# Kernel tuning notes

Measured on AMD Instinct MI355X. Metric: run time of the kernel, lower is better.

The kernel has to match this reference:

```python
import jax, jax.numpy as jnp
import numpy as np
import math

B, S_IMG, S_TXT = 1, 2048, 256
D_MODEL, HEADS, HEAD_DIM = 3072, 24, 128
INNER = HEADS * HEAD_DIM
EPS = 1e-6


def _rmsnorm(x, scale):
    # flax-style RMSNorm over last dim, fp32 stats
    x32 = x.astype(jnp.float32)
    var = jnp.mean(x32 * x32, axis=-1, keepdims=True)
    return ((x32 * jax.lax.rsqrt(var + EPS)).astype(x.dtype)) * scale


def _rope(x, cos, sin):
    # x: [B,S,H,D]; cos,sin: [S,D]; interleaved-pair rotation (use_real_unbind_dim=-1)
    c = cos[None, :, None, :].astype(jnp.float32)
    s = sin[None, :, None, :].astype(jnp.float32)
    xp = x.reshape(*x.shape[:-1], -1, 2)
    x_rot = jnp.stack([-xp[..., 1], xp[..., 0]], axis=-1).reshape(x.shape)
    return (x.astype(jnp.float32) * c + x_rot.astype(jnp.float32) * s).astype(x.dtype)


def setup_inputs() -> dict:
    key = jax.random.key(0)
    ks = jax.random.split(key, 16)
    w = lambda k, shp: jax.random.normal(k, shp, jnp.float32) * 0.02
    S = S_TXT + S_IMG
    pos = jnp.arange(S, dtype=jnp.float32)
    inv_freq = 1.0 / (10000.0 ** (jnp.arange(0, HEAD_DIM, 2, dtype=jnp.float32) / HEAD_DIM))
    ang = pos[:, None] * inv_freq[None, :]  # [S, D/2]
    cos = jnp.repeat(jnp.cos(ang), 2, axis=-1)  # [S, D] paired layout
    sin = jnp.repeat(jnp.sin(ang), 2, axis=-1)
    return {
        'hidden_states': jax.random.normal(ks[0], (B, S_IMG, D_MODEL), jnp.float32),
        'encoder_hidden_states': jax.random.normal(ks[1], (B, S_TXT, D_MODEL), jnp.float32),
        'cos': cos,
        'sin': sin,
        'wq': w(ks[2], (D_MODEL, INNER)),
        'wk': w(ks[3], (D_MODEL, INNER)),
        'wv': w(ks[4], (D_MODEL, INNER)),
        'wq_add': w(ks[5], (D_MODEL, INNER)),
        'wk_add': w(ks[6], (D_MODEL, INNER)),
        'wv_add': w(ks[7], (D_MODEL, INNER)),
        'bq_add': w(ks[8], (INNER,)),
        'bk_add': w(ks[9], (INNER,)),
        'bv_add': w(ks[10], (INNER,)),
        'norm_q': jnp.ones((HEAD_DIM,), jnp.float32),
        'norm_k': jnp.ones((HEAD_DIM,), jnp.float32),
        'norm_add_q': jnp.ones((HEAD_DIM,), jnp.float32),
        'norm_add_k': jnp.ones((HEAD_DIM,), jnp.float32),
        'w_out': w(ks[11], (INNER, D_MODEL)),
        'b_out': w(ks[12], (D_MODEL,)),
        'w_add_out': w(ks[13], (INNER, D_MODEL)),
        'b_add_out': w(ks[14], (D_MODEL,)),
    }


def reference(hidden_states, encoder_hidden_states, cos, sin, wq, wk, wv,
              wq_add, wk_add, wv_add, bq_add, bk_add, bv_add,
              norm_q, norm_k, norm_add_q, norm_add_k,
              w_out, b_out, w_add_out, b_add_out):
    St = encoder_hidden_states.shape[1]
    heads = lambda x: x.reshape(x.shape[0], x.shape[1], HEADS, HEAD_DIM)
    # image-token q/k/v + QK RMSNorm
    q = _rmsnorm(heads(hidden_states @ wq), norm_q)
    k = _rmsnorm(heads(hidden_states @ wk), norm_k)
    v = heads(hidden_states @ wv)
    # encoder-token q/k/v (biased projections) + QK RMSNorm
    eq = _rmsnorm(heads(encoder_hidden_states @ wq_add + bq_add), norm_add_q)
    ek = _rmsnorm(heads(encoder_hidden_states @ wk_add + bk_add), norm_add_k)
    ev = heads(encoder_hidden_states @ wv_add + bv_add)
    # encoder tokens concatenated first
    q = jnp.concatenate([eq, q], axis=1)
    k = jnp.concatenate([ek, k], axis=1)
    v = jnp.concatenate([ev, v], axis=1)
    q = _rope(q, cos, sin)
    k = _rope(k, cos, sin)
    # naive softmax attention
    scale = 1.0 / math.sqrt(HEAD_DIM)
    attn = jnp.einsum('bshd,bthd->bhst', q, k) * scale
    attn = jax.nn.softmax(attn, axis=-1)
    out = jnp.einsum('bhst,bthd->bshd', attn, v)
    out = out.reshape(out.shape[0], out.shape[1], -1)
    # split back into encoder / image streams and apply output projections
    enc_out = out[:, :St] @ w_add_out + b_add_out
    img_out = out[:, St:] @ w_out + b_out
    return (img_out, enc_out)
```

## Files before the change

kernel.cpp:

```cpp
#include <hip/hip_runtime.h>
#include <hip/hip_bf16.h>

typedef unsigned short u16;
typedef unsigned int   u32;
typedef __bf16 bf16x8 __attribute__((ext_vector_type(8)));
typedef float  f32x4  __attribute__((ext_vector_type(4)));

#define SEQ   2304
#define DM    3072
#define NH    24
#define HD    128
#define S_TXT 256
#define S_IMG 2048
#define SCALE 0.08838834764831845f

__device__ __forceinline__ u16 f2bf(float x) {
  u32 u = __float_as_uint(x);
  u += 0x7fffu + ((u >> 16) & 1u);
  return (u16)(u >> 16);
}
__device__ __forceinline__ float bf2f(u16 b) {
  return __uint_as_float(((u32)b) << 16);
}
__device__ __forceinline__ f32x4 zero4() { f32x4 z = {0.f, 0.f, 0.f, 0.f}; return z; }

#define GLDS16(gp, lp) __builtin_amdgcn_global_load_lds( \
    (__attribute__((address_space(1))) void*)(gp),       \
    (__attribute__((address_space(3))) void*)(lp), 16, 0, 0)

__global__ __launch_bounds__(256) void conv_bf16_k(const float* __restrict__ src,
                                                   u16* __restrict__ dst, int n4) {
  int i = blockIdx.x * 256 + threadIdx.x;
  if (i >= n4) return;
  float4 v = ((const float4*)src)[i];
  ushort4 o;
  o.x = f2bf(v.x); o.y = f2bf(v.y); o.z = f2bf(v.z); o.w = f2bf(v.w);
  ((ushort4*)dst)[i] = o;
}

struct WP { const float* s[8]; u16* d[8]; };

__global__ __launch_bounds__(256) void w_transpose_k(WP p) {
  __shared__ float tile[32][33];
  const float* __restrict__ src = p.s[blockIdx.z];
  u16* __restrict__ dst = p.d[blockIdx.z];
  const int c0 = blockIdx.x * 32, r0 = blockIdx.y * 32;
  const int tx = threadIdx.x & 31, ty = threadIdx.x >> 5;
#pragma unroll
  for (int i = 0; i < 4; ++i)
    tile[ty + i*8][tx] = src[(size_t)(r0 + ty + i*8) * DM + c0 + tx];
  __syncthreads();
#pragma unroll
  for (int i = 0; i < 4; ++i)
    dst[(size_t)(c0 + ty + i*8) * DM + r0 + tx] = f2bf(tile[tx][ty + i*8]);
}

__global__ __launch_bounds__(256) void v_transpose_k(const u16* __restrict__ V,
                                                     u16* __restrict__ Vt) {
  __shared__ u16 tile[32][34];
  const int h = blockIdx.z;
  const int t0 = blockIdx.x * 32, d0 = blockIdx.y * 32;
  const int tx = threadIdx.x & 31, ty = threadIdx.x >> 5;
#pragma unroll
  for (int i = 0; i < 4; ++i)
    tile[ty + i*8][tx] = V[((size_t)h * SEQ + t0 + ty + i*8) * HD + d0 + tx];
  __syncthreads();
#pragma unroll
  for (int i = 0; i < 4; ++i)
    Vt[((size_t)h * HD + d0 + ty + i*8) * SEQ + t0 + tx] = tile[tx][ty + i*8];
}

__global__ __launch_bounds__(256) void gemm_bt_k(
    const u16* __restrict__ A,
    const u16* __restrict__ B0, const u16* __restrict__ B1, const u16* __restrict__ B2,
    const float* __restrict__ bias0, const float* __restrict__ bias1, const float* __restrict__ bias2,
    void* __restrict__ out0, void* __restrict__ out1, void* __restrict__ out2,
    int row_off, int mode) {
  __shared__ __attribute__((aligned(128))) char As[128*128];
  __shared__ __attribute__((aligned(128))) char Bs[128*128];
  const int bz = blockIdx.z;
  const u16* __restrict__ Bm = (bz == 0) ? B0 : ((bz == 1) ? B1 : B2);
  const float* __restrict__ bias = (bz == 0) ? bias0 : ((bz == 1) ? bias1 : bias2);
  void* out = (bz == 0) ? out0 : ((bz == 1) ? out1 : out2);
  const int bm = blockIdx.x, bn = blockIdx.y;
  const int tid = threadIdx.x;
  const int w = tid >> 6, l = tid & 63;
  const int wr = w >> 1, wc = w & 1;

  f32x4 acc[4][4];
#pragma unroll
  for (int mi = 0; mi < 4; ++mi)
#pragma unroll
    for (int ni = 0; ni < 4; ++ni) acc[mi][ni] = zero4();

  const int srow  = l >> 3;
  const int scolb = ((l & 7) ^ srow) << 4;
  const char* Ag = (const char*)(A  + (size_t)(bm*128 + w*32) * DM) + (size_t)srow * (DM*2) + scolb;
  const char* Bg = (const char*)(Bm + (size_t)(bn*128 + w*32) * DM) + (size_t)srow * (DM*2) + scolb;
  char* AsW = As + (w*32) * 128;
  char* BsW = Bs + (w*32) * 128;

  for (int kt = 0; kt < DM/64; ++kt) {
#pragma unroll
    for (int i = 0; i < 4; ++i) {
      GLDS16(Ag + (size_t)i*8*(DM*2) + kt*128, AsW + i*8*128);
      GLDS16(Bg + (size_t)i*8*(DM*2) + kt*128, BsW + i*8*128);
    }
    __syncthreads();
#pragma unroll
    for (int kk = 0; kk < 2; ++kk) {
      bf16x8 af[4], bfr[4];
#pragma unroll
      for (int mi = 0; mi < 4; ++mi) {
        const int row = wr*64 + mi*16 + (l & 15);
        const int cb  = ((kk << 6) + ((l >> 4) << 4)) ^ ((row & 7) << 4);
        af[mi] = *(const bf16x8*)(As + row*128 + cb);
      }
#pragma unroll
      for (int ni = 0; ni < 4; ++ni) {
        const int row = wc*64 + ni*16 + (l & 15);
        const int cb  = ((kk << 6) + ((l >> 4) << 4)) ^ ((row & 7) << 4);
        bfr[ni] = *(const bf16x8*)(Bs + row*128 + cb);
      }
#pragma unroll
      for (int mi = 0; mi < 4; ++mi)
#pragma unroll
        for (int ni = 0; ni < 4; ++ni)
          acc[mi][ni] = __builtin_amdgcn_mfma_f32_16x16x32_bf16(af[mi], bfr[ni], acc[mi][ni], 0, 0, 0);
    }
    __syncthreads();
  }

#pragma unroll
  for (int mi = 0; mi < 4; ++mi) {
    const int mbase = bm*128 + wr*64 + mi*16 + ((l >> 4) << 2);
#pragma unroll
    for (int ni = 0; ni < 4; ++ni) {
      const int ncol = bn*128 + wc*64 + ni*16 + (l & 15);
      const float bv = bias ? bias[ncol] : 0.f;
#pragma unroll
      for (int r = 0; r < 4; ++r) {
        const float v = acc[mi][ni][r] + bv;
        if (mode == 0) {
          ((u16*)out)[((size_t)bn * SEQ + (row_off + mbase + r)) * HD + (ncol & 127)] = f2bf(v);
        } else {
          ((float*)out)[(size_t)(mbase + r) * DM + ncol] = v;
        }
      }
    }
  }
}

__global__ __launch_bounds__(256) void qk_norm_rope_k(
    const u16* __restrict__ Qf, const u16* __restrict__ Kf,
    u16* __restrict__ Qb, u16* __restrict__ Kb,
    const float* __restrict__ cosT, const float* __restrict__ sinT,
    const float* __restrict__ nq, const float* __restrict__ nk,
    const float* __restrict__ naq, const float* __restrict__ nak) {
  const int gw = (blockIdx.x * 256 + threadIdx.x) >> 6;
  const int l = threadIdx.x & 63;
  const int which = (gw >= NH * SEQ) ? 1 : 0;
  const int rem = which ? (gw - NH * SEQ) : gw;
  const int h = rem / SEQ, t = rem % SEQ;
  const size_t base = ((size_t)h * SEQ + t) * HD + l * 2;
  const ushort2 xb = *(const ushort2*)((which ? Kf : Qf) + base);
  const float x0 = bf2f(xb.x), x1 = bf2f(xb.y);
  float ss = x0*x0 + x1*x1;
#pragma unroll
  for (int msk = 1; msk < 64; msk <<= 1) ss += __shfl_xor(ss, msk, 64);
  const float rr = rsqrtf(ss * (1.0f/128.0f) + 1e-6f);
  const float* nw = which ? (t < S_TXT ? nak : nk) : (t < S_TXT ? naq : nq);
  const float n0 = x0 * rr * nw[l*2], n1 = x1 * rr * nw[l*2 + 1];
  const float c = cosT[(size_t)t * HD + l*2], sn = sinT[(size_t)t * HD + l*2];
  float o0 = n0 * c - n1 * sn;
  float o1 = n1 * c + n0 * sn;
  if (!which) { o0 *= SCALE; o1 *= SCALE; }
  ushort2 ob; ob.x = f2bf(o0); ob.y = f2bf(o1);
  *(ushort2*)((which ? Kb : Qb) + base) = ob;
}

__global__ __launch_bounds__(256) void attn_k(
    const u16* __restrict__ Q, const u16* __restrict__ K,
    const u16* __restrict__ Vt, u16* __restrict__ O) {
  __shared__ __attribute__((aligned(128))) char Kl[64*256];
  __shared__ __attribute__((aligned(128))) char Vl[128*128];
  __shared__ __attribute__((aligned(128))) char Pl[4][2048];
  const int qt = blockIdx.x, h = blockIdx.y;
  const int tid = threadIdx.x, w = tid >> 6, l = tid & 63;

  const u16* Qh = Q  + ((size_t)h * SEQ + qt*64 + w*16) * HD;
  const u16* Kh = K  + (size_t)h * SEQ * HD;
  const u16* Vh = Vt + (size_t)h * HD * SEQ;

  bf16x8 qf[4];
#pragma unroll
  for (int kf = 0; kf < 4; ++kf)
    qf[kf] = *(const bf16x8*)(Qh + (l & 15) * HD + kf*32 + ((l >> 4) << 3));

  f32x4 o[8];
#pragma unroll
  for (int db = 0; db < 8; ++db) o[db] = zero4();
  float m[4]  = {-1e30f, -1e30f, -1e30f, -1e30f};
  float rl[4] = {0.f, 0.f, 0.f, 0.f};

  const int vswz = ((l & 7) ^ (l >> 3)) << 4;

  for (int kb = 0; kb < SEQ/64; ++kb) {
#pragma unroll
    for (int i = 0; i < 4; ++i) {
      const int rloc = i*4 + (l >> 4);
      const int colb = ((l & 15) << 4) ^ ((rloc & 7) << 4);
      GLDS16((const char*)Kh + ((size_t)(kb*64 + w*16 + rloc)) * 256 + colb,
             Kl + (w*16 + i*4) * 256);
    }
#pragma unroll
    for (int i = 0; i < 4; ++i) {
      const int rloc = w*32 + i*8 + (l >> 3);
      GLDS16((const char*)Vh + (size_t)rloc * (SEQ*2) + kb*128 + vswz,
             Vl + (w*32 + i*8) * 128);
    }
    __syncthreads();

    f32x4 s[4];
#pragma unroll
    for (int ni = 0; ni < 4; ++ni) {
      f32x4 a = zero4();
      const int row = ni*16 + (l & 15);
#pragma unroll
      for (int kf = 0; kf < 4; ++kf) {
        const int cb = ((kf << 6) + ((l >> 4) << 4)) ^ ((row & 7) << 4);
        bf16x8 kfr = *(const bf16x8*)(Kl + row*256 + cb);
        a = __builtin_amdgcn_mfma_f32_16x16x32_bf16(qf[kf], kfr, a, 0, 0, 0);
      }
      s[ni] = a;
    }

    float mnew[4], resc[4];
#pragma unroll
    for (int r = 0; r < 4; ++r) {
      float mx = fmaxf(fmaxf(s[0][r], s[1][r]), fmaxf(s[2][r], s[3][r]));
#pragma unroll
      for (int msk = 1; msk < 16; msk <<= 1) mx = fmaxf(mx, __shfl_xor(mx, msk, 64));
      mnew[r] = fmaxf(m[r], mx);
      resc[r] = __expf(m[r] - mnew[r]);
      m[r] = mnew[r];
    }
#pragma unroll
    for (int ni = 0; ni < 4; ++ni) {
      f32x4 t = s[ni];
#pragma unroll
      for (int r = 0; r < 4; ++r) t[r] = __expf(t[r] - m[r]);
      s[ni] = t;
    }
#pragma unroll
    for (int r = 0; r < 4; ++r) {
      float t = s[0][r] + s[1][r] + s[2][r] + s[3][r];
#pragma unroll
      for (int msk = 1; msk < 16; msk <<= 1) t += __shfl_xor(t, msk, 64);
      rl[r] = rl[r] * resc[r] + t;
    }
#pragma unroll
    for (int db = 0; db < 8; ++db) {
      f32x4 t = o[db];
#pragma unroll
      for (int r = 0; r < 4; ++r) t[r] *= resc[r];
      o[db] = t;
    }

    char* Pw = Pl[w];
#pragma unroll
    for (int ni = 0; ni < 4; ++ni)
#pragma unroll
      for (int r = 0; r < 4; ++r) {
        const int prow = ((l >> 4) << 2) + r;
        const int pcb  = ((ni*16 + (l & 15)) << 1) ^ ((prow & 7) << 4);
        *(u16*)(Pw + prow*128 + pcb) = f2bf(s[ni][r]);
      }

    const int arow = l & 15;
#pragma unroll
    for (int kblk = 0; kblk < 2; ++kblk) {
      const int pcb = ((kblk << 6) + ((l >> 4) << 4)) ^ ((arow & 7) << 4);
      bf16x8 pa = *(const bf16x8*)(Pw + arow*128 + pcb);
#pragma unroll
      for (int db = 0; db < 8; ++db) {
        const int vrow = db*16 + (l & 15);
        const int vcb  = ((kblk << 6) + ((l >> 4) << 4)) ^ ((vrow & 7) << 4);
        bf16x8 vb = *(const bf16x8*)(Vl + vrow*128 + vcb);
        o[db] = __builtin_amdgcn_mfma_f32_16x16x32_bf16(pa, vb, o[db], 0, 0, 0);
      }
    }
    __syncthreads();
  }

#pragma unroll
  for (int r = 0; r < 4; ++r) rl[r] = 1.f / rl[r];
#pragma unroll
  for (int db = 0; db < 8; ++db)
#pragma unroll
    for (int r = 0; r < 4; ++r) {
      const int token = qt*64 + w*16 + ((l >> 4) << 2) + r;
      const int col = h*HD + db*16 + (l & 15);
      O[(size_t)token * DM + col] = f2bf(o[db][r] * rl[r]);
    }
}

extern "C" void kernel_launch(void* const* d_in, const int* in_sizes, int n_in,
                              void* d_out, int out_size, void* d_ws, size_t ws_size,
                              hipStream_t stream) {
  const float* hidden = (const float*)d_in[0];
  const float* ench   = (const float*)d_in[1];
  const float* cosT   = (const float*)d_in[2];
  const float* sinT   = (const float*)d_in[3];
  const float* wq  = (const float*)d_in[4];
  const float* wk  = (const float*)d_in[5];
  const float* wv  = (const float*)d_in[6];
  const float* wqa = (const float*)d_in[7];
  const float* wka = (const float*)d_in[8];
  const float* wva = (const float*)d_in[9];
  const float* bqa = (const float*)d_in[10];
  const float* bka = (const float*)d_in[11];
  const float* bva = (const float*)d_in[12];
  const float* nq  = (const float*)d_in[13];
  const float* nk  = (const float*)d_in[14];
  const float* naq = (const float*)d_in[15];
  const float* nak = (const float*)d_in[16];
  const float* w_out     = (const float*)d_in[17];
  const float* b_out     = (const float*)d_in[18];
  const float* w_add_out = (const float*)d_in[19];
  const float* b_add_out = (const float*)d_in[20];
  float* outp = (float*)d_out;
  (void)in_sizes; (void)n_in; (void)out_size; (void)ws_size;

  char* ws = (char*)d_ws;
  size_t off = 0;
  auto alloc = [&](size_t n) { char* p = ws + off; off += (n + 255) & ~(size_t)255; return p; };
  u16* wt[8];
  for (int i = 0; i < 8; ++i) wt[i] = (u16*)alloc((size_t)DM * DM * 2);
  u16* xb_img = (u16*)alloc((size_t)S_IMG * DM * 2);
  u16* xb_enc = (u16*)alloc((size_t)S_TXT * DM * 2);
  u16* Qf = (u16*)alloc((size_t)NH * SEQ * HD * 2);
  u16* Kf = (u16*)alloc((size_t)NH * SEQ * HD * 2);
  u16* Vf = (u16*)alloc((size_t)NH * SEQ * HD * 2);
  u16* Qb = (u16*)alloc((size_t)NH * SEQ * HD * 2);
  u16* Kb = (u16*)alloc((size_t)NH * SEQ * HD * 2);
  u16* Vt = (u16*)alloc((size_t)NH * HD * SEQ * 2);
  u16* Ob = (u16*)alloc((size_t)SEQ * DM * 2);

  conv_bf16_k<<<(S_IMG*DM/4)/256, 256, 0, stream>>>(hidden, xb_img, S_IMG*DM/4);
  conv_bf16_k<<<(S_TXT*DM/4)/256, 256, 0, stream>>>(ench, xb_enc, S_TXT*DM/4);

  WP wp;
  wp.s[0] = wq;  wp.s[1] = wk;  wp.s[2] = wv;
  wp.s[3] = wqa; wp.s[4] = wka; wp.s[5] = wva;
  wp.s[6] = w_out; wp.s[7] = w_add_out;
  for (int i = 0; i < 8; ++i) wp.d[i] = wt[i];
  w_transpose_k<<<dim3(96, 96, 8), 256, 0, stream>>>(wp);

  gemm_bt_k<<<dim3(16, 24, 3), 256, 0, stream>>>(xb_img, wt[0], wt[1], wt[2],
      nullptr, nullptr, nullptr, Qf, Kf, Vf, S_TXT, 0);
  gemm_bt_k<<<dim3(2, 24, 3), 256, 0, stream>>>(xb_enc, wt[3], wt[4], wt[5],
      bqa, bka, bva, Qf, Kf, Vf, 0, 0);

  qk_norm_rope_k<<<(2*NH*SEQ)/4, 256, 0, stream>>>(Qf, Kf, Qb, Kb, cosT, sinT, nq, nk, naq, nak);
  v_transpose_k<<<dim3(SEQ/32, HD/32, NH), 256, 0, stream>>>(Vf, Vt);

  attn_k<<<dim3(SEQ/64, NH), 256, 0, stream>>>(Qb, Kb, Vt, Ob);

  gemm_bt_k<<<dim3(16, 24, 1), 256, 0, stream>>>(Ob + (size_t)S_TXT * DM, wt[6], wt[6], wt[6],
      b_out, b_out, b_out, outp, outp, outp, 0, 1);
  gemm_bt_k<<<dim3(2, 24, 1), 256, 0, stream>>>(Ob, wt[7], wt[7], wt[7],
      b_add_out, b_add_out, b_add_out,
      outp + (size_t)S_IMG * DM, outp + (size_t)S_IMG * DM, outp + (size_t)S_IMG * DM, 0, 1);
}
```

Before: 939.7 us.

## Process two query tiles per wave in attention to reuse K/V LDS loads

Each wave now handles 32 query rows (two 16-row tiles) instead of 16, so each block covers 128 queries and the grid is halved. Every K and V fragment read from LDS now feeds two MFMAs. QK^T is computed transposed (K as the A operand), so the row max and row sum need only two cross-lane shuffles. P is packed with v_cvt_pk_bf16_f32. This cuts LDS and global K/V traffic per query but raises register pressure, and the smaller grid (18x24 blocks) may lower occupancy and CU fill.

```diff
diff --git a/kernel.cpp b/kernel.cpp
--- a/kernel.cpp
+++ b/kernel.cpp
@@ -23,6 +23,11 @@
   return __uint_as_float(((u32)b) << 16);
 }
 __device__ __forceinline__ f32x4 zero4() { f32x4 z = {0.f, 0.f, 0.f, 0.f}; return z; }
+__device__ __forceinline__ u32 cvtpk(float lo, float hi) {
+  u32 r;
+  asm("v_cvt_pk_bf16_f32 %0, %1, %2" : "=v"(r) : "v"(lo), "v"(hi));
+  return r;
+}
 
 #define GLDS16(gp, lp) __builtin_amdgcn_global_load_lds( \
     (__attribute__((address_space(1))) void*)(gp),       \
@@ -184,26 +189,32 @@
     const u16* __restrict__ Vt, u16* __restrict__ O) {
   __shared__ __attribute__((aligned(128))) char Kl[64*256];
   __shared__ __attribute__((aligned(128))) char Vl[128*128];
-  __shared__ __attribute__((aligned(128))) char Pl[4][2048];
-  const int qt = blockIdx.x, h = blockIdx.y;
+  __shared__ __attribute__((aligned(128))) char Pl[4][2][2048];
+  const int qb = blockIdx.x, h = blockIdx.y;
   const int tid = threadIdx.x, w = tid >> 6, l = tid & 63;
-
-  const u16* Qh = Q  + ((size_t)h * SEQ + qt*64 + w*16) * HD;
+  const int g = l >> 4, q16 = l & 15;
+
+  const u16* Qh = Q  + ((size_t)h * SEQ + qb*128 + w*32) * HD;
   const u16* Kh = K  + (size_t)h * SEQ * HD;
   const u16* Vh = Vt + (size_t)h * HD * SEQ;
 
-  bf16x8 qf[4];
-#pragma unroll
-  for (int kf = 0; kf < 4; ++kf)
-    qf[kf] = *(const bf16x8*)(Qh + (l & 15) * HD + kf*32 + ((l >> 4) << 3));
-
-  f32x4 o[8];
-#pragma unroll
-  for (int db = 0; db < 8; ++db) o[db] = zero4();
-  float m[4]  = {-1e30f, -1e30f, -1e30f, -1e30f};
-  float rl[4] = {0.f, 0.f, 0.f, 0.f};
+  bf16x8 qf[2][4];
+#pragma unroll
+  for (int qt = 0; qt < 2; ++qt)
+#pragma unroll
+    for (int kf = 0; kf < 4; ++kf)
+      qf[qt][kf] = *(const bf16x8*)(Qh + (qt*16 + q16) * HD + kf*32 + g*8);
+
+  f32x4 o[2][8];
+#pragma unroll
+  for (int qt = 0; qt < 2; ++qt)
+#pragma unroll
+    for (int db = 0; db < 8; ++db) o[qt][db] = zero4();
+  float m[2]  = {-3e38f, -3e38f};
+  float rl[2] = {0.f, 0.f};
 
   const int vswz = ((l & 7) ^ (l >> 3)) << 4;
+  const int pswz = (q16 & 7) << 4;
 
   for (int kb = 0; kb < SEQ/64; ++kb) {
 #pragma unroll
@@ -221,88 +232,111 @@
     }
     __syncthreads();
 
-    f32x4 s[4];
-#pragma unroll
-    for (int ni = 0; ni < 4; ++ni) {
-      f32x4 a = zero4();
-      const int row = ni*16 + (l & 15);
+    f32x4 s[2][4];
+#pragma unroll
+    for (int qt = 0; qt < 2; ++qt)
+#pragma unroll
+      for (int mi = 0; mi < 4; ++mi) s[qt][mi] = zero4();
+#pragma unroll
+    for (int mi = 0; mi < 4; ++mi) {
+      const int row = mi*16 + q16;
+      bf16x8 kfr[4];
 #pragma unroll
       for (int kf = 0; kf < 4; ++kf) {
-        const int cb = ((kf << 6) + ((l >> 4) << 4)) ^ ((row & 7) << 4);
-        bf16x8 kfr = *(const bf16x8*)(Kl + row*256 + cb);
-        a = __builtin_amdgcn_mfma_f32_16x16x32_bf16(qf[kf], kfr, a, 0, 0, 0);
-      }
-      s[ni] = a;
-    }
-
-    float mnew[4], resc[4];
-#pragma unroll
-    for (int r = 0; r < 4; ++r) {
-      float mx = fmaxf(fmaxf(s[0][r], s[1][r]), fmaxf(s[2][r], s[3][r]));
-#pragma unroll
-      for (int msk = 1; msk < 16; msk <<= 1) mx = fmaxf(mx, __shfl_xor(mx, msk, 64));
-      mnew[r] = fmaxf(m[r], mx);
-      resc[r] = __expf(m[r] - mnew[r]);
-      m[r] = mnew[r];
-    }
-#pragma unroll
-    for (int ni = 0; ni < 4; ++ni) {
-      f32x4 t = s[ni];
-#pragma unroll
-      for (int r = 0; r < 4; ++r) t[r] = __expf(t[r] - m[r]);
-      s[ni] = t;
-    }
-#pragma unroll
-    for (int r = 0; r < 4; ++r) {
-      float t = s[0][r] + s[1][r] + s[2][r] + s[3][r];
-#pragma unroll
-      for (int msk = 1; msk < 16; msk <<= 1) t += __shfl_xor(t, msk, 64);
-      rl[r] = rl[r] * resc[r] + t;
-    }
-#pragma unroll
-    for (int db = 0; db < 8; ++db) {
-      f32x4 t = o[db];
-#pragma unroll
-      for (int r = 0; r < 4; ++r) t[r] *= resc[r];
-      o[db] = t;
-    }
-
-    char* Pw = Pl[w];
-#pragma unroll
-    for (int ni = 0; ni < 4; ++ni)
-#pragma unroll
-      for (int r = 0; r < 4; ++r) {
-        const int prow = ((l >> 4) << 2) + r;
-        const int pcb  = ((ni*16 + (l & 15)) << 1) ^ ((prow & 7) << 4);
-        *(u16*)(Pw + prow*128 + pcb) = f2bf(s[ni][r]);
-      }
-
-    const int arow = l & 15;
-#pragma unroll
-    for (int kblk = 0; kblk < 2; ++kblk) {
-      const int pcb = ((kblk << 6) + ((l >> 4) << 4)) ^ ((arow & 7) << 4);
-      bf16x8 pa = *(const bf16x8*)(Pw + arow*128 + pcb);
+        const int cb = ((kf << 6) + (g << 4)) ^ ((row & 7) << 4);
+        kfr[kf] = *(const bf16x8*)(Kl + row*256 + cb);
+      }
+#pragma unroll
+      for (int kf = 0; kf < 4; ++kf) {
+        s[0][mi] = __builtin_amdgcn_mfma_f32_16x16x32_bf16(kfr[kf], qf[0][kf], s[0][mi], 0, 0, 0);
+        s[1][mi] = __builtin_amdgcn_mfma_f32_16x16x32_bf16(kfr[kf], qf[1][kf], s[1][mi], 0, 0, 0);
+      }
+    }
+
+    float rsv[2];
+#pragma unroll
+    for (int qt = 0; qt < 2; ++qt) {
+      float mx = s[qt][0][0];
+#pragma unroll
+      for (int mi = 0; mi < 4; ++mi)
+#pragma unroll
+        for (int r = 0; r < 4; ++r) mx = fmaxf(mx, s[qt][mi][r]);
+      mx = fmaxf(mx, __shfl_xor(mx, 16, 64));
+      mx = fmaxf(mx, __shfl_xor(mx, 32, 64));
+      const float mn = fmaxf(m[qt], mx);
+      rsv[qt] = __expf(m[qt] - mn);
+      m[qt] = mn;
+      float sum = 0.f;
+#pragma unroll
+      for (int mi = 0; mi < 4; ++mi) {
+        f32x4 t = s[qt][mi];
+#pragma unroll
+        for (int r = 0; r < 4; ++r) { t[r] = __expf(t[r] - mn); sum += t[r]; }
+        s[qt][mi] = t;
+      }
+      sum += __shfl_xor(sum, 16, 64);
+      sum += __shfl_xor(sum, 32, 64);
+      rl[qt] = rl[qt] * rsv[qt] + sum;
+      char* Pw = Pl[w][qt];
+#pragma unroll
+      for (int mi = 0; mi < 4; ++mi) {
+        uint2 pk;
+        pk.x = cvtpk(s[qt][mi][0], s[qt][mi][1]);
+        pk.y = cvtpk(s[qt][mi][2], s[qt][mi][3]);
+        *(uint2*)(Pw + ((q16*128 + mi*32 + g*8) ^ pswz)) = pk;
+      }
+    }
+
+#pragma unroll
+    for (int qt = 0; qt < 2; ++qt) {
+      float rs4[4];
+#pragma unroll
+      for (int r = 0; r < 4; ++r)
+        rs4[r] = __shfl(rsv[qt], (g << 4) + (g << 2) + r, 64);
 #pragma unroll
       for (int db = 0; db < 8; ++db) {
-        const int vrow = db*16 + (l & 15);
-        const int vcb  = ((kblk << 6) + ((l >> 4) << 4)) ^ ((vrow & 7) << 4);
+        f32x4 t = o[qt][db];
+#pragma unroll
+        for (int r = 0; r < 4; ++r) t[r] *= rs4[r];
+        o[qt][db] = t;
+      }
+    }
+
+    bf16x8 pa[2][2];
+#pragma unroll
+    for (int qt = 0; qt < 2; ++qt)
+#pragma unroll
+      for (int kblk = 0; kblk < 2; ++kblk)
+        pa[qt][kblk] = *(const bf16x8*)(Pl[w][qt] + ((q16*128 + kblk*64 + g*16) ^ pswz));
+
+#pragma unroll
+    for (int kblk = 0; kblk < 2; ++kblk)
+#pragma unroll
+      for (int db = 0; db < 8; ++db) {
+        const int vrow = db*16 + q16;
+        const int vcb  = ((kblk << 6) + (g << 4)) ^ ((vrow & 7) << 4);
         bf16x8 vb = *(const bf16x8*)(Vl + vrow*128 + vcb);
-        o[db] = __builtin_amdgcn_mfma_f32_16x16x32_bf16(pa, vb, o[db], 0, 0, 0);
-      }
-    }
+        o[0][db] = __builtin_amdgcn_mfma_f32_16x16x32_bf16(pa[0][kblk], vb, o[0][db], 0, 0, 0);
+        o[1][db] = __builtin_amdgcn_mfma_f32_16x16x32_bf16(pa[1][kblk], vb, o[1][db], 0, 0, 0);
+      }
     __syncthreads();
   }
 
 #pragma unroll
-  for (int r = 0; r < 4; ++r) rl[r] = 1.f / rl[r];
-#pragma unroll
-  for (int db = 0; db < 8; ++db)
-#pragma unroll
-    for (int r = 0; r < 4; ++r) {
-      const int token = qt*64 + w*16 + ((l >> 4) << 2) + r;
-      const int col = h*HD + db*16 + (l & 15);
-      O[(size_t)token * DM + col] = f2bf(o[db][r] * rl[r]);
-    }
+  for (int qt = 0; qt < 2; ++qt) {
+    float inv4[4];
+#pragma unroll
+    for (int r = 0; r < 4; ++r)
+      inv4[r] = 1.f / __shfl(rl[qt], (g << 4) + (g << 2) + r, 64);
+#pragma unroll
+    for (int db = 0; db < 8; ++db)
+#pragma unroll
+      for (int r = 0; r < 4; ++r) {
+        const int token = qb*128 + w*32 + qt*16 + g*4 + r;
+        const int col = h*HD + db*16 + q16;
+        O[(size_t)token * DM + col] = f2bf(o[qt][db][r] * inv4[r]);
+      }
+  }
 }
 
 extern "C" void kernel_launch(void* const* d_in, const int* in_sizes, int n_in,
@@ -365,7 +399,7 @@
   qk_norm_rope_k<<<(2*NH*SEQ)/4, 256, 0, stream>>>(Qf, Kf, Qb, Kb, cosT, sinT, nq, nk, naq, nak);
   v_transpose_k<<<dim3(SEQ/32, HD/32, NH), 256, 0, stream>>>(Vf, Vt);
 
-  attn_k<<<dim3(SEQ/64, NH), 256, 0, stream>>>(Qb, Kb, Vt, Ob);
+  attn_k<<<dim3(SEQ/128, NH), 256, 0, stream>>>(Qb, Kb, Vt, Ob);
 
   gemm_bt_k<<<dim3(16, 24, 1), 256, 0, stream>>>(Ob + (size_t)S_TXT * DM, wt[6], wt[6], wt[6],
       b_out, b_out, b_out, outp, outp, outp, 0, 1);
```

New measurement: 937.8 us. About the same (-0.2%).
